# Kernel tuning notes

Measured on AMD Instinct MI355X. Metric: run time of the kernel, lower is better.

Reference implementation:

```python
import jax, jax.numpy as jnp
import numpy as np

EPS = 1e-5  # torch BatchNorm default eps


def _bn(x, gamma, beta, axes):
    # training-mode batch norm over `axes` (channel axis is 1), biased variance as in torch
    mean = x.mean(axis=axes, keepdims=True)
    var = x.var(axis=axes, keepdims=True)
    shp = [1] * x.ndim
    shp[1] = -1
    return gamma.reshape(shp) * (x - mean) * jax.lax.rsqrt(var + EPS) + beta.reshape(shp)


def setup_inputs() -> dict:
    key = jax.random.key(0)
    k0, k1, k2 = jax.random.split(key, 3)
    B, C, H, W = 4, 64, 128, 128
    OP2 = 128      # out_planes * 2
    HEAD = 8       # head_dim
    HP = OP2 // HEAD  # head_planes = 16
    return {
        "x": jax.random.normal(k0, (B, C, H, W), jnp.float32),
        "w_qkv": jax.random.normal(k1, (OP2, C), jnp.float32) / np.sqrt(C).astype(np.float32),
        "gamma1": jnp.ones((OP2,), jnp.float32),
        "beta1": jnp.zeros((OP2,), jnp.float32),
        "pos_relative": jax.random.normal(k2, (HP, 2 * H - 1), jnp.float32) / np.sqrt(C).astype(np.float32),
        "gate_qr": jnp.array([0.1], jnp.float32),
        "gate_kr": jnp.array([0.1], jnp.float32),
        "gate_v_pos": jnp.array([0.1], jnp.float32),
        "gate_v": jnp.array([1.0], jnp.float32),
        "gamma_att": jnp.ones((3 * HEAD,), jnp.float32),
        "beta_att": jnp.zeros((3 * HEAD,), jnp.float32),
        "gamma_v": jnp.ones((2 * HEAD,), jnp.float32),
        "beta_v": jnp.zeros((2 * HEAD,), jnp.float32),
    }


def reference(x, w_qkv, gamma1, beta1, pos_relative, gate_qr, gate_kr,
              gate_v_pos, gate_v, gamma_att, beta_att, gamma_v, beta_v):
    b, c, H, W = x.shape
    # h_w='h': permute [0,3,1,2] -> (b, W, c, H), fuse (b, W)
    xp = jnp.transpose(x, (0, 3, 1, 2)).reshape(b * W, c, H)  # [N, c, H]
    # to_qkv: 1x1 Conv1d (no bias) + ReLU + BatchNorm1d (training mode)
    y = jax.nn.relu(jnp.einsum('oc,ncl->nol', w_qkv, xp))      # [N, 2*out_planes, H]
    y = _bn(y, gamma1, beta1, (0, 2))

    head_dim = gamma_att.shape[0] // 3
    hp = y.shape[1] // head_dim          # head_planes
    qk_dim = hp // 4
    v_dim = hp // 2
    qkv = y.reshape(-1, head_dim, hp, H)  # [N, head_dim, head_planes, H]
    q = qkv[:, :, :qk_dim]
    k = qkv[:, :, qk_dim:2 * qk_dim]
    v = qkv[:, :, 2 * qk_dim:]

    # relative-position gather: pos_relative[:, q_idx - k_idx + H - 1] -> [head_planes, H, H]
    rel = jnp.arange(H)[:, None] - jnp.arange(H)[None, :] + H - 1
    qk_pos = pos_relative[:, rel]
    q_pos = qk_pos[:qk_dim]
    k_pos = qk_pos[qk_dim:2 * qk_dim]
    v_pos = qk_pos[2 * qk_dim:]

    qk = jnp.einsum('nhcp,nhci->nhpi', q, k)                 # [N, head_dim, H, H]
    qr = jnp.einsum('nhcp,cpi->nhpi', q, q_pos) * gate_qr
    kr = jnp.einsum('nhcp,cpi->nhpi', k, k_pos) * gate_kr

    att = _bn(jnp.concatenate([qk, qr, kr], axis=1), gamma_att, beta_att, (0, 2, 3))
    att = att.reshape(-1, 3, head_dim, H, H).sum(axis=1)
    att = jax.nn.softmax(att, axis=-1)

    att_v = jnp.einsum('nhpi,nhci->nhcp', att, v * gate_v)          # [N, head_dim, v_dim, H]
    att_vp = jnp.einsum('nhpi,cpi->nhcp', att, v_pos * gate_v_pos)

    z = _bn(jnp.concatenate([att_v, att_vp], axis=1), gamma_v, beta_v, (0, 2, 3))
    z = z.reshape(b, W, 2, head_dim * v_dim, H).sum(axis=2)  # [b, W, out_planes, H]
    # h_w='h': permute [0,2,3,1] -> (b, out_planes, H, W)
    return jnp.transpose(z, (0, 2, 3, 1))
```

## Files before the change

kernel.cpp:

```cpp
#include <hip/hip_runtime.h>
#include <hip/hip_fp16.h>

#define EPS 1e-5f



typedef _Float16 half2_t __attribute__((ext_vector_type(2)));

__device__ __constant__ int pair_c [10] = {0,0,0,0,1,1,1,2,2,3};
__device__ __constant__ int pair_cp[10] = {0,1,2,3,1,2,3,2,3,3};

__device__ inline float fdot2(half2_t a, half2_t b, float c) {
#if __has_builtin(__builtin_amdgcn_fdot2)
  return __builtin_amdgcn_fdot2(a, b, c, false);
#else
  return c + (float)a[0] * (float)b[0] + (float)a[1] * (float)b[1];
#endif
}
__device__ inline half2_t bch2(unsigned u) {
  union { unsigned u; half2_t h; } x; x.u = u; return x.h;
}
__device__ inline unsigned packf2(float a, float b) {
  half2_t h; h[0] = (_Float16)a; h[1] = (_Float16)b;
  union { unsigned u; half2_t h; } x; x.h = h; return x.u;
}

__global__ __launch_bounds__(256) void k1_gemm(
    const float* __restrict__ x, const float* __restrict__ wq,
    _Float16* __restrict__ y1h, float* __restrict__ Pbuf)
{
  __shared__ float xs[64][132];
  const int b = blockIdx.x >> 7, l = blockIdx.x & 127;
  const int tid = threadIdx.x;
  const float* xp = x + (size_t)b * 1048576 + (size_t)l * 128;
  for (int idx = tid; idx < 8192; idx += 256) {
    int c = idx >> 7, wv = idx & 127;
    xs[c][wv] = xp[c * 16384 + wv];
  }
  __syncthreads();
  const int ty = tid >> 4, tx = tid & 15;
  const int o0 = ty * 8, w0 = tx * 4;
  float acc[8][8];
#pragma unroll
  for (int u = 0; u < 8; ++u)
#pragma unroll
    for (int v = 0; v < 8; ++v) acc[u][v] = 0.f;

  for (int c4 = 0; c4 < 64; c4 += 4) {
    float wr[8][4];
#pragma unroll
    for (int u = 0; u < 8; ++u)
      *(float4*)&wr[u][0] = *(const float4*)&wq[(o0 + u) * 64 + c4];
#pragma unroll
    for (int dc = 0; dc < 4; ++dc) {
      float4 xa = *(const float4*)&xs[c4 + dc][w0];
      float4 xb = *(const float4*)&xs[c4 + dc][w0 + 64];
#pragma unroll
      for (int u = 0; u < 8; ++u) {
        float wv = wr[u][dc];
        acc[u][0] += wv * xa.x; acc[u][1] += wv * xa.y;
        acc[u][2] += wv * xa.z; acc[u][3] += wv * xa.w;
        acc[u][4] += wv * xb.x; acc[u][5] += wv * xb.y;
        acc[u][6] += wv * xb.z; acc[u][7] += wv * xb.w;
      }
    }
  }
  _Float16* y1p = y1h + (size_t)(b * 128 + l) * 16384;
#pragma unroll
  for (int u = 0; u < 8; ++u) {
#pragma unroll
    for (int v = 0; v < 8; ++v) acc[u][v] = fmaxf(acc[u][v], 0.f);
    uint2 pa, pb;
    pa.x = packf2(acc[u][0], acc[u][1]); pa.y = packf2(acc[u][2], acc[u][3]);
    pb.x = packf2(acc[u][4], acc[u][5]); pb.y = packf2(acc[u][6], acc[u][7]);
    *(uint2*)&y1p[(o0 + u) * 128 + w0] = pa;
    *(uint2*)&y1p[(o0 + u) * 128 + w0 + 64] = pb;
    float s  = acc[u][0] + acc[u][1] + acc[u][2] + acc[u][3]
             + acc[u][4] + acc[u][5] + acc[u][6] + acc[u][7];
    float ss = acc[u][0]*acc[u][0] + acc[u][1]*acc[u][1] + acc[u][2]*acc[u][2]
             + acc[u][3]*acc[u][3] + acc[u][4]*acc[u][4] + acc[u][5]*acc[u][5]
             + acc[u][6]*acc[u][6] + acc[u][7]*acc[u][7];
#pragma unroll
    for (int off = 1; off < 16; off <<= 1) {
      s  += __shfl_xor(s, off);
      ss += __shfl_xor(ss, off);
    }
    if (tx == 0) {
      Pbuf[blockIdx.x * 256 + o0 + u] = s;
      Pbuf[blockIdx.x * 256 + 128 + o0 + u] = ss;
    }
  }
}

__global__ __launch_bounds__(64) void k2_bn1(
    const float* __restrict__ Pbuf, float* __restrict__ S,
    const float* __restrict__ g1, const float* __restrict__ b1)
{
  const int t = blockIdx.x;
  const int lane = threadIdx.x;
  float s1 = 0.f, s2 = 0.f;
#pragma unroll
  for (int m = 0; m < 8; ++m) {
    int blk = lane + 64 * m;
    s1 += Pbuf[blk * 256 + t];
    s2 += Pbuf[blk * 256 + 128 + t];
  }
#pragma unroll
  for (int off = 1; off < 64; off <<= 1) {
    s1 += __shfl_xor(s1, off);
    s2 += __shfl_xor(s2, off);
  }
  if (lane == 0) {
    const float inv = 1.f / 65536.f;
    float m = s1 * inv;
    float var = s2 * inv - m * m;
    float sc = g1[t] * rsqrtf(var + EPS);
    S[256 + t] = sc;
    S[384 + t] = b1[t] - m * sc;
  }
}

__global__ __launch_bounds__(256) void k_tr(
    const _Float16* __restrict__ y1h, const float* __restrict__ S,
    unsigned* __restrict__ y2h)
{
  __shared__ _Float16 th[2][64][134];
  const int s = blockIdx.x & 63, b = blockIdx.x >> 6;
  const int h = s >> 3, slot = s & 7;
  const int o0 = 2 * s, o1 = 2 * s + 1;
  const float sc0 = S[256 + o0], sh0 = S[384 + o0];
  const float sc1 = S[256 + o1], sh1 = S[384 + o1];
  const int tid = threadIdx.x;
  for (int lh = 0; lh < 2; ++lh) {
    const int l0 = lh * 64;
    for (int idx = tid; idx < 4096; idx += 256) {
      int ll = idx >> 6, wp = idx & 63;
      size_t base = ((size_t)(b * 128 + l0 + ll) * 128) * 128 + 2 * wp;
      unsigned a0 = *(const unsigned*)&y1h[base + (size_t)o0 * 128];
      unsigned a1 = *(const unsigned*)&y1h[base + (size_t)o1 * 128];
      half2_t ha = bch2(a0), hb = bch2(a1);
      *(unsigned*)&th[0][ll][2 * wp] =
          packf2((float)ha[0] * sc0 + sh0, (float)ha[1] * sc0 + sh0);
      *(unsigned*)&th[1][ll][2 * wp] =
          packf2((float)hb[0] * sc1 + sh1, (float)hb[1] * sc1 + sh1);
    }
    __syncthreads();
    for (int idx = tid; idx < 8192; idx += 256) {
      int w = idx >> 6, ll = idx & 63;
      unsigned pk;
      { half2_t hh; hh[0] = th[0][ll][w]; hh[1] = th[1][ll][w];
        union { unsigned u; half2_t h; } xx; xx.h = hh; pk = xx.u; }
      y2h[((size_t)((b * 128 + w) * 8 + h) * 8 + slot) * 128 + l0 + ll] = pk;
    }
    __syncthreads();
  }
}

__global__ __launch_bounds__(128) void k0_pos(const float* __restrict__ pos,
                                              float* __restrict__ PT,
                                              unsigned* __restrict__ pos_h,
                                              unsigned* __restrict__ vpxg)
{
  const int blk = blockIdx.x, tid = threadIdx.x;
  if (blk == 28) {
    for (int u = tid; u < 255; u += 128) {
#pragma unroll
      for (int s = 0; s < 4; ++s)
        pos_h[u * 4 + s] = packf2(pos[(2 * s) * 255 + u], pos[(2 * s + 1) * 255 + u]);
    }
    return;
  }
  if (blk == 29) {
    for (int m = tid; m < 3072; m += 128) {
      int sel = m / 1536, rem = m % 1536, rp = rem / 12, c = rem % 12;
      unsigned val = 0;
      if (c < 8) {
        int ua = (sel ? 254 : 253) - 2 * rp;
        int ub = ua - 1;
        float fa = (ua >= 0) ? pos[(8 + c) * 255 + ua] : 0.f;
        float fb = (ub >= 0) ? pos[(8 + c) * 255 + ub] : 0.f;
        val = packf2(fa, fb);
      }
      vpxg[m] = val;
    }
    return;
  }
  __shared__ float r0[255], r1[255];
  int rowA, rowB, out;
  bool prod;
  if (blk < 4)       { rowA = blk;                 rowB = rowA;               out = blk * 128;              prod = false; }
  else if (blk < 14) { int m = blk - 4;  rowA = pair_c[m];     rowB = pair_cp[m];     out = 1024 + m * 128; prod = true; }
  else if (blk < 18) { rowA = 4 + (blk - 14);      rowB = rowA;               out = 512 + (blk - 14) * 128; prod = false; }
  else               { int m = blk - 18; rowA = 4 + pair_c[m]; rowB = 4 + pair_cp[m]; out = 2304 + m * 128; prod = true; }
  for (int u = tid; u < 255; u += 128) {
    r0[u] = pos[rowA * 255 + u];
    r1[u] = pos[rowB * 255 + u];
  }
  __syncthreads();
  float s = 0.f;
  if (prod) {
    for (int d = 0; d < 128; ++d) s += r0[tid + d] * r1[tid + d];
  } else {
    for (int d = 0; d < 128; ++d) s += r0[tid + d];
  }
  PT[out + tid] = s;
}

__global__ __launch_bounds__(256) void k3_stats(
    const unsigned* __restrict__ y2h, const float* __restrict__ PT,
    float* __restrict__ Pb3)
{
  const int W = blockIdx.x * 4 + (threadIdx.x >> 6);
  const int lane = threadIdx.x & 63;
  const int h = W & 7;
  const int n0 = (W >> 3) * 8;
  float Pq[4][2], Pk[4][2], Wq[10][2], Wk[10][2];
#pragma unroll
  for (int c = 0; c < 4; ++c) {
    Pq[c][0] = PT[c * 128 + lane];        Pq[c][1] = PT[c * 128 + 64 + lane];
    Pk[c][0] = PT[512 + c * 128 + lane];  Pk[c][1] = PT[512 + c * 128 + 64 + lane];
  }
#pragma unroll
  for (int m = 0; m < 10; ++m) {
    Wq[m][0] = PT[1024 + m * 128 + lane]; Wq[m][1] = PT[1024 + m * 128 + 64 + lane];
    Wk[m][0] = PT[2304 + m * 128 + lane]; Wk[m][1] = PT[2304 + m * 128 + 64 + lane];
  }
  float acc_qk = 0, acc_qkss = 0, acc_qr = 0, acc_qrss = 0, acc_kr = 0, acc_krss = 0;
  for (int t = 0; t < 8; ++t) {
    const unsigned* yb = y2h + (size_t)((n0 + t) * 8 + h) * 1024;
    float q[4][2], k[4][2];
#pragma unroll
    for (int pl = 0; pl < 2; ++pl) {
      half2_t ha = bch2(yb[pl * 128 + lane]);
      half2_t hb = bch2(yb[pl * 128 + 64 + lane]);
      q[2 * pl][0] = (float)ha[0]; q[2 * pl + 1][0] = (float)ha[1];
      q[2 * pl][1] = (float)hb[0]; q[2 * pl + 1][1] = (float)hb[1];
      half2_t hc = bch2(yb[(2 + pl) * 128 + lane]);
      half2_t hd = bch2(yb[(2 + pl) * 128 + 64 + lane]);
      k[2 * pl][0] = (float)hc[0]; k[2 * pl + 1][0] = (float)hc[1];
      k[2 * pl][1] = (float)hd[0]; k[2 * pl + 1][1] = (float)hd[1];
    }
#pragma unroll
    for (int c = 0; c < 4; ++c) {
      acc_qr += q[c][0] * Pq[c][0] + q[c][1] * Pq[c][1];
      acc_kr += k[c][0] * Pk[c][0] + k[c][1] * Pk[c][1];
    }
#pragma unroll
    for (int m = 0; m < 10; ++m) {
      int c = pair_c[m], cp = pair_cp[m];
      float mult = (c == cp) ? 1.f : 2.f;
      acc_qrss += mult * (q[c][0] * q[cp][0] * Wq[m][0] + q[c][1] * q[cp][1] * Wq[m][1]);
      acc_krss += mult * (k[c][0] * k[cp][0] * Wk[m][0] + k[c][1] * k[cp][1] * Wk[m][1]);
    }
    float vals[28];
#pragma unroll
    for (int c = 0; c < 4; ++c) {
      vals[c]     = q[c][0] + q[c][1];
      vals[4 + c] = k[c][0] + k[c][1];
    }
#pragma unroll
    for (int m = 0; m < 10; ++m) {
      int c = pair_c[m], cp = pair_cp[m];
      vals[8 + m]  = q[c][0] * q[cp][0] + q[c][1] * q[cp][1];
      vals[18 + m] = k[c][0] * k[cp][0] + k[c][1] * k[cp][1];
    }
#pragma unroll
    for (int v = 0; v < 28; ++v) {
      float tv = vals[v];
#pragma unroll
      for (int off = 1; off < 64; off <<= 1) tv += __shfl_xor(tv, off);
      vals[v] = tv;
    }
    float qk = 0, qkss = 0;
#pragma unroll
    for (int c = 0; c < 4; ++c) qk += vals[c] * vals[4 + c];
#pragma unroll
    for (int m = 0; m < 10; ++m) {
      float mult = (pair_c[m] == pair_cp[m]) ? 1.f : 2.f;
      qkss += mult * vals[8 + m] * vals[18 + m];
    }
    acc_qk += qk; acc_qkss += qkss;
  }
  float lin[4] = {acc_qr, acc_qrss, acc_kr, acc_krss};
#pragma unroll
  for (int v = 0; v < 4; ++v) {
    float tv = lin[v];
#pragma unroll
    for (int off = 1; off < 64; off <<= 1) tv += __shfl_xor(tv, off);
    lin[v] = tv;
  }
  if (lane == 0) {
    float* o = Pb3 + W * 6;
    o[0] = acc_qk; o[1] = acc_qkss;
    o[2] = lin[0]; o[3] = lin[1]; o[4] = lin[2]; o[5] = lin[3];
  }
}

__global__ __launch_bounds__(64) void kR1(
    const float* __restrict__ Pb3, float* __restrict__ S,
    const float* __restrict__ ga, const float* __restrict__ ba,
    const float* __restrict__ gqr, const float* __restrict__ gkr)
{
  __shared__ float sums[48];
  const int t = threadIdx.x;
  if (t < 48) {
    int h = t / 6, k = t % 6;
    float v = 0.f;
    for (int g = 0; g < 64; ++g) v += Pb3[(h + 8 * g) * 6 + k];
    sums[t] = v;
  }
  __syncthreads();
  if (t < 8) {
    const int h = t;
    const float inv = 1.f / 8388608.f;
    float gates[3] = {1.f, gqr[0], gkr[0]};
    float csum = 0.f;
#pragma unroll
    for (int g = 0; g < 3; ++g) {
      float mr = sums[h * 6 + 2 * g] * inv;
      float er = sums[h * 6 + 2 * g + 1] * inv;
      float gt = gates[g];
      float mean = gt * mr;
      float var = gt * gt * er - mean * mean;
      float sc = ga[g * 8 + h] * rsqrtf(var + EPS);
      S[560 + g * 8 + h] = gt * sc;
      csum += ba[g * 8 + h] - mean * sc;
    }
    S[584 + h] = csum;
  }
}

__global__ __launch_bounds__(512, 6) void k5_apply(
    const unsigned* __restrict__ y2h, const unsigned* __restrict__ pos_h,
    const unsigned* __restrict__ vpxg,
    float* __restrict__ S, _Float16* __restrict__ av, _Float16* __restrict__ avp,
    const float* __restrict__ gv_p, const float* __restrict__ gvp_p,
    float* __restrict__ Vbuf)
{
  __shared__ __align__(16) unsigned qkv_s[128][4];
  __shared__ __align__(16) unsigned posm[255][4];
  __shared__ __align__(16) unsigned vt[64][8];
  __shared__ __align__(16) unsigned vpx[2][128][12];
  __shared__ float red[8][4];
  const int h = blockIdx.x & 7, n = blockIdx.x >> 3;
  const int tid = threadIdx.x;
  const unsigned* yb = y2h + (size_t)(n * 8 + h) * 1024;
  {
    int l = tid >> 2, s = tid & 3;
    qkv_s[l][s] = yb[s * 128 + l];
  }
  {
    unsigned* pf = (unsigned*)posm;
    for (int m = tid; m < 1020; m += 512) pf[m] = pos_h[m];
  }
  {
    unsigned* pf = (unsigned*)vpx;
    for (int m = tid; m < 3072; m += 512) pf[m] = vpxg[m];
  }
  if (tid < 256) {
    int s = tid & 3, jp = tid >> 2;
    unsigned a0 = yb[(4 + s) * 128 + 2 * jp];
    unsigned a1 = yb[(4 + s) * 128 + 2 * jp + 1];
    vt[jp][2 * s]     = (a0 & 0xffffu) | (a1 << 16);
    vt[jp][2 * s + 1] = (a0 >> 16) | (a1 & 0xffff0000u);
  }
  __syncthreads();

  const int p = tid >> 2, isub = tid & 3;
  uint2 qk2 = *(const uint2*)&qkv_s[p][0];
  uint2 kown = *(const uint2*)&qkv_s[p][2];
  const half2_t q01 = bch2(qk2.x), q23 = bch2(qk2.y);
  const half2_t k01o = bch2(kown.x), k23o = bch2(kown.y);
  const float C0 = S[560 + h], C1 = S[568 + h], C2 = S[576 + h], C3v = S[584 + h];
  const unsigned* vprow = &vpx[p & 1][63 - (p >> 1)][0];

  float mcur = -1e30f;
  float sum = 0.f;
  float accv[8], accvp[8];
#pragma unroll
  for (int c = 0; c < 8; ++c) { accv[c] = 0.f; accvp[c] = 0.f; }

#pragma unroll 4
  for (int j = 0; j < 16; ++j) {
    const int jp = isub + 4 * j;
    const int i0 = 2 * jp;
    const int u0 = p - i0 + 127;
    uint2 ka = *(const uint2*)&qkv_s[i0][2];
    uint2 kb = *(const uint2*)&qkv_s[i0 + 1][2];
    uint4 pa = *(const uint4*)&posm[u0][0];
    uint4 pb = *(const uint4*)&posm[u0 - 1][0];
    float aa0 = fdot2(q23, bch2(ka.y), fdot2(q01, bch2(ka.x), 0.f));
    float bq0 = fdot2(q23, bch2(pa.y), fdot2(q01, bch2(pa.x), 0.f));
    float ckA = fdot2(k23o, bch2(pa.w), fdot2(k01o, bch2(pa.z), 0.f));
    float aa1 = fdot2(q23, bch2(kb.y), fdot2(q01, bch2(kb.x), 0.f));
    float bq1 = fdot2(q23, bch2(pb.y), fdot2(q01, bch2(pb.x), 0.f));
    float ckB = fdot2(k23o, bch2(pb.w), fdot2(k01o, bch2(pb.z), 0.f));
    float s0 = aa0 * C0 + bq0 * C1 + ckA * C2 + C3v;
    float s1 = aa1 * C0 + bq1 * C1 + ckB * C2 + C3v;
    float mp = fmaxf(s0, s1);
    if (mp > mcur) {
      float r = __expf(mcur - mp);
      mcur = mp;
      sum *= r;
#pragma unroll
      for (int c = 0; c < 8; ++c) { accv[c] *= r; accvp[c] *= r; }
    }
    float e0 = __expf(s0 - mcur);
    float e1 = __expf(s1 - mcur);
    sum += e0 + e1;
    const half2_t e2 = bch2(packf2(e0, e1));
    uint4 va = *(const uint4*)&vt[jp][0];
    uint4 vb = *(const uint4*)&vt[jp][4];
    const unsigned* wr = vprow + jp * 12;
    uint4 wa = *(const uint4*)wr;
    uint4 wb = *(const uint4*)(wr + 4);
    accv[0] = fdot2(e2, bch2(va.x), accv[0]);
    accv[1] = fdot2(e2, bch2(va.y), accv[1]);
    accv[2] = fdot2(e2, bch2(va.z), accv[2]);
    accv[3] = fdot2(e2, bch2(va.w), accv[3]);
    accv[4] = fdot2(e2, bch2(vb.x), accv[4]);
    accv[5] = fdot2(e2, bch2(vb.y), accv[5]);
    accv[6] = fdot2(e2, bch2(vb.z), accv[6]);
    accv[7] = fdot2(e2, bch2(vb.w), accv[7]);
    accvp[0] = fdot2(e2, bch2(wa.x), accvp[0]);
    accvp[1] = fdot2(e2, bch2(wa.y), accvp[1]);
    accvp[2] = fdot2(e2, bch2(wa.z), accvp[2]);
    accvp[3] = fdot2(e2, bch2(wa.w), accvp[3]);
    accvp[4] = fdot2(e2, bch2(wb.x), accvp[4]);
    accvp[5] = fdot2(e2, bch2(wb.y), accvp[5]);
    accvp[6] = fdot2(e2, bch2(wb.z), accvp[6]);
    accvp[7] = fdot2(e2, bch2(wb.w), accvp[7]);
  }
  float M = fmaxf(mcur, __shfl_xor(mcur, 1));
  M = fmaxf(M, __shfl_xor(M, 2));
  {
    float r = __expf(mcur - M);
    sum *= r;
#pragma unroll
    for (int c = 0; c < 8; ++c) { accv[c] *= r; accvp[c] *= r; }
  }
  sum += __shfl_xor(sum, 1);
  sum += __shfl_xor(sum, 2);
#pragma unroll
  for (int c = 0; c < 8; ++c) {
    accv[c]  += __shfl_xor(accv[c], 1);  accv[c]  += __shfl_xor(accv[c], 2);
    accvp[c] += __shfl_xor(accvp[c], 1); accvp[c] += __shfl_xor(accvp[c], 2);
  }

  float sv = 0, ssv = 0, svp = 0, ssvp = 0;
  if (isub == 0) {
    const float fv = gv_p[0] / sum, fp2 = gvp_p[0] / sum;
    size_t base = ((size_t)(n * 8 + h) * 8) * 128 + p;
#pragma unroll
    for (int c = 0; c < 8; ++c) {
      float x1 = accv[c] * fv;
      float x2 = accvp[c] * fp2;
      av [base + c * 128] = (_Float16)x1;
      avp[base + c * 128] = (_Float16)x2;
      sv += x1; ssv += x1 * x1; svp += x2; ssvp += x2 * x2;
    }
  }
  float vals[4] = {sv, ssv, svp, ssvp};
#pragma unroll
  for (int kk = 0; kk < 4; ++kk) {
    float v = vals[kk];
#pragma unroll
    for (int off = 1; off < 64; off <<= 1) v += __shfl_xor(v, off);
    vals[kk] = v;
  }
  const int wid = tid >> 6, lane = tid & 63;
  if (lane == 0) {
#pragma unroll
    for (int kk = 0; kk < 4; ++kk) red[wid][kk] = vals[kk];
  }
  __syncthreads();
  if (tid == 0) {
    float t0 = 0, t1 = 0, t2 = 0, t3 = 0;
#pragma unroll
    for (int w = 0; w < 8; ++w) {
      t0 += red[w][0]; t1 += red[w][1]; t2 += red[w][2]; t3 += red[w][3];
    }
    float* o = Vbuf + (size_t)blockIdx.x * 4;
    o[0] = t0; o[1] = t1; o[2] = t2; o[3] = t3;
  }
}

__global__ __launch_bounds__(512) void kR2(
    const float* __restrict__ Vbuf, float* __restrict__ S,
    const float* __restrict__ gv, const float* __restrict__ bv)
{
  __shared__ float part[32][17];
  const int t = threadIdx.x;
  const int col = t >> 4, sub = t & 15;
  const int k = col >> 3, h = col & 7;
  float v = 0.f;
  for (int m = 0; m < 32; ++m) {
    int n = sub + 16 * m;
    v += Vbuf[(size_t)(n * 8 + h) * 4 + k];
  }
  part[col][sub] = v;
  __syncthreads();
  if (t < 32) {
    float s = 0.f;
#pragma unroll
    for (int j = 0; j < 16; ++j) s += part[t][j];
    part[t][16] = s;
  }
  __syncthreads();
  if (t < 8) {
    const int hh = t;
    const float inv = 1.f / 524288.f;
    float m1 = part[0 * 8 + hh][16] * inv;
    float e1 = part[1 * 8 + hh][16] * inv;
    float var = e1 - m1 * m1;
    float sc = gv[hh] * rsqrtf(var + EPS);
    S[624 + hh] = sc;
    S[632 + hh] = bv[hh] - m1 * sc;
    float m2 = part[2 * 8 + hh][16] * inv;
    float e2 = part[3 * 8 + hh][16] * inv;
    var = e2 - m2 * m2;
    sc = gv[8 + hh] * rsqrtf(var + EPS);
    S[640 + hh] = sc;
    S[648 + hh] = bv[8 + hh] - m2 * sc;
  }
}

__global__ __launch_bounds__(256) void k7_out(
    const _Float16* __restrict__ av, const _Float16* __restrict__ avp,
    const float* __restrict__ S, float* __restrict__ out)
{
  __shared__ float tile[64][129];
  const int wt = blockIdx.x & 1;
  const int d  = (blockIdx.x >> 1) & 63;
  const int b  = blockIdx.x >> 7;
  const int h = d >> 3, c = d & 7;
  const float scv = S[624 + h], shv = S[632 + h];
  const float scp = S[640 + h], shp = S[648 + h];
  const int tid = threadIdx.x;
  for (int idx = tid; idx < 8192; idx += 256) {
    int wl = idx >> 7, pp = idx & 127;
    int n = b * 128 + wt * 64 + wl;
    size_t base = (((size_t)n * 8 + h) * 8 + c) * 128 + pp;
    tile[wl][pp] = (float)av[base] * scv + shv + (float)avp[base] * scp + shp;
  }
  __syncthreads();
  for (int idx = tid; idx < 8192; idx += 256) {
    int pp = idx >> 6, wl = idx & 63;
    out[(((size_t)b * 64 + d) * 128 + pp) * 128 + wt * 64 + wl] = tile[wl][pp];
  }
}

extern "C" void kernel_launch(void* const* d_in, const int* in_sizes, int n_in,
                              void* d_out, int out_size, void* d_ws, size_t ws_size,
                              hipStream_t stream)
{
  const float* x   = (const float*)d_in[0];
  const float* wq  = (const float*)d_in[1];
  const float* g1  = (const float*)d_in[2];
  const float* b1  = (const float*)d_in[3];
  const float* pos = (const float*)d_in[4];
  const float* gqr = (const float*)d_in[5];
  const float* gkr = (const float*)d_in[6];
  const float* gvp = (const float*)d_in[7];
  const float* gv  = (const float*)d_in[8];
  const float* ga  = (const float*)d_in[9];
  const float* ba  = (const float*)d_in[10];
  const float* gv2 = (const float*)d_in[11];
  const float* bv2 = (const float*)d_in[12];

  float* ws = (float*)d_ws;
  _Float16* y1h   = (_Float16*)ws;
  _Float16* av    = (_Float16*)ws;
  _Float16* avp   = (_Float16*)ws + 4194304;
  float*    Pb3   = ws + 4200000;
  float*    Vbuf  = ws + 4250000;
  float*    Pbuf  = ws + 8388608;
  unsigned* y2h   = (unsigned*)(ws + 8388608);
  float*    S     = ws + 16777216;
  unsigned* pos_h = (unsigned*)(ws + 16778240);
  float*    PT    = ws + 16781312;
  unsigned* vpxg  = (unsigned*)(ws + 16785000);
  float*    out   = (float*)d_out;

  k0_pos<<<30, 128, 0, stream>>>(pos, PT, pos_h, vpxg);
  k1_gemm<<<512, 256, 0, stream>>>(x, wq, y1h, Pbuf);
  k2_bn1<<<128, 64, 0, stream>>>(Pbuf, S, g1, b1);
  k_tr<<<256, 256, 0, stream>>>(y1h, S, y2h);
  k3_stats<<<128, 256, 0, stream>>>(y2h, PT, Pb3);
  kR1<<<1, 64, 0, stream>>>(Pb3, S, ga, ba, gqr, gkr);
  k5_apply<<<4096, 512, 0, stream>>>(y2h, pos_h, vpxg, S, av, avp, gv, gvp, Vbuf);
  kR2<<<1, 512, 0, stream>>>(Vbuf, S, gv2, bv2);
  k7_out<<<512, 256, 0, stream>>>(av, avp, S, out);
}
```

Before: 215.7 us.

## Fuse BN1 finalize into transpose, vectorize x loads, widen softmax inner loop

Removes the separate k2_bn1 launch: each k_tr block now reduces the BN1 partial sums for its two channels itself and computes scale and shift locally. Pbuf is moved to a different workspace offset, presumably so it no longer overlaps y2h, which k_tr now writes while still reading Pbuf. The k1_gemm shared-memory fill now uses float4 loads, and the k5_apply attention loop handles four scores per iteration with paired fdot2 accumulation and a dot-with-ones for the running sum. The trade is redundant BN1 reductions across the 4 batch blocks per channel pair and higher register pressure in the fully unrolled attention loop.

```diff
diff --git a/kernel.cpp b/kernel.cpp
--- a/kernel.cpp
+++ b/kernel.cpp
@@ -33,9 +33,9 @@
   const int b = blockIdx.x >> 7, l = blockIdx.x & 127;
   const int tid = threadIdx.x;
   const float* xp = x + (size_t)b * 1048576 + (size_t)l * 128;
-  for (int idx = tid; idx < 8192; idx += 256) {
-    int c = idx >> 7, wv = idx & 127;
-    xs[c][wv] = xp[c * 16384 + wv];
+  for (int idx = tid; idx < 2048; idx += 256) {
+    int c = idx >> 5, w4 = (idx & 31) * 4;
+    *(float4*)&xs[c][w4] = *(const float4*)&xp[c * 16384 + w4];
   }
   __syncthreads();
   const int ty = tid >> 4, tx = tid & 15;
@@ -92,45 +92,33 @@
   }
 }
 
-__global__ __launch_bounds__(64) void k2_bn1(
-    const float* __restrict__ Pbuf, float* __restrict__ S,
-    const float* __restrict__ g1, const float* __restrict__ b1)
-{
-  const int t = blockIdx.x;
-  const int lane = threadIdx.x;
-  float s1 = 0.f, s2 = 0.f;
-#pragma unroll
-  for (int m = 0; m < 8; ++m) {
-    int blk = lane + 64 * m;
-    s1 += Pbuf[blk * 256 + t];
-    s2 += Pbuf[blk * 256 + 128 + t];
-  }
-#pragma unroll
-  for (int off = 1; off < 64; off <<= 1) {
-    s1 += __shfl_xor(s1, off);
-    s2 += __shfl_xor(s2, off);
-  }
-  if (lane == 0) {
-    const float inv = 1.f / 65536.f;
-    float m = s1 * inv;
-    float var = s2 * inv - m * m;
-    float sc = g1[t] * rsqrtf(var + EPS);
-    S[256 + t] = sc;
-    S[384 + t] = b1[t] - m * sc;
-  }
-}
-
 __global__ __launch_bounds__(256) void k_tr(
-    const _Float16* __restrict__ y1h, const float* __restrict__ S,
+    const _Float16* __restrict__ y1h, const float* __restrict__ Pbuf,
+    const float* __restrict__ g1, const float* __restrict__ b1,
     unsigned* __restrict__ y2h)
 {
   __shared__ _Float16 th[2][64][134];
+  __shared__ float scsh[4];
   const int s = blockIdx.x & 63, b = blockIdx.x >> 6;
   const int h = s >> 3, slot = s & 7;
   const int o0 = 2 * s, o1 = 2 * s + 1;
-  const float sc0 = S[256 + o0], sh0 = S[384 + o0];
-  const float sc1 = S[256 + o1], sh1 = S[384 + o1];
   const int tid = threadIdx.x;
+  {
+    int r = tid >> 6, lane = tid & 63;
+    int row = ((r & 1) ? o1 : o0) + (r >> 1) * 128;
+    float a = 0.f;
+#pragma unroll
+    for (int m = 0; m < 8; ++m) a += Pbuf[(lane + 64 * m) * 256 + row];
+#pragma unroll
+    for (int off = 1; off < 64; off <<= 1) a += __shfl_xor(a, off);
+    if (lane == 0) scsh[r] = a;
+  }
+  __syncthreads();
+  const float inv = 1.f / 65536.f;
+  const float m0 = scsh[0] * inv, v0 = scsh[2] * inv - m0 * m0;
+  const float m1 = scsh[1] * inv, v1 = scsh[3] * inv - m1 * m1;
+  const float sc0 = g1[o0] * rsqrtf(v0 + EPS), sh0 = b1[o0] - m0 * sc0;
+  const float sc1 = g1[o1] * rsqrtf(v1 + EPS), sh1 = b1[o1] - m1 * sc1;
   for (int lh = 0; lh < 2; ++lh) {
     const int l0 = lh * 64;
     for (int idx = tid; idx < 4096; idx += 256) {
@@ -373,6 +361,7 @@
   const half2_t k01o = bch2(kown.x), k23o = bch2(kown.y);
   const float C0 = S[560 + h], C1 = S[568 + h], C2 = S[576 + h], C3v = S[584 + h];
   const unsigned* vprow = &vpx[p & 1][63 - (p >> 1)][0];
+  const half2_t one2 = bch2(packf2(1.f, 1.f));
 
   float mcur = -1e30f;
   float sum = 0.f;
@@ -380,24 +369,34 @@
 #pragma unroll
   for (int c = 0; c < 8; ++c) { accv[c] = 0.f; accvp[c] = 0.f; }
 
-#pragma unroll 4
-  for (int j = 0; j < 16; ++j) {
-    const int jp = isub + 4 * j;
-    const int i0 = 2 * jp;
-    const int u0 = p - i0 + 127;
-    uint2 ka = *(const uint2*)&qkv_s[i0][2];
-    uint2 kb = *(const uint2*)&qkv_s[i0 + 1][2];
-    uint4 pa = *(const uint4*)&posm[u0][0];
-    uint4 pb = *(const uint4*)&posm[u0 - 1][0];
-    float aa0 = fdot2(q23, bch2(ka.y), fdot2(q01, bch2(ka.x), 0.f));
-    float bq0 = fdot2(q23, bch2(pa.y), fdot2(q01, bch2(pa.x), 0.f));
-    float ckA = fdot2(k23o, bch2(pa.w), fdot2(k01o, bch2(pa.z), 0.f));
-    float aa1 = fdot2(q23, bch2(kb.y), fdot2(q01, bch2(kb.x), 0.f));
-    float bq1 = fdot2(q23, bch2(pb.y), fdot2(q01, bch2(pb.x), 0.f));
-    float ckB = fdot2(k23o, bch2(pb.w), fdot2(k01o, bch2(pb.z), 0.f));
-    float s0 = aa0 * C0 + bq0 * C1 + ckA * C2 + C3v;
-    float s1 = aa1 * C0 + bq1 * C1 + ckB * C2 + C3v;
-    float mp = fmaxf(s0, s1);
+#pragma unroll
+  for (int jj = 0; jj < 8; ++jj) {
+    const int jpA = isub + 8 * jj;
+    const int jpB = jpA + 4;
+    const int i0A = 2 * jpA, i0B = 2 * jpB;
+    const int uA = p - i0A + 127;
+    const int uB = uA - 8;
+    uint2 kaA = *(const uint2*)&qkv_s[i0A][2];
+    uint2 kbA = *(const uint2*)&qkv_s[i0A + 1][2];
+    uint2 kaB = *(const uint2*)&qkv_s[i0B][2];
+    uint2 kbB = *(const uint2*)&qkv_s[i0B + 1][2];
+    uint4 paA = *(const uint4*)&posm[uA][0];
+    uint4 pbA = *(const uint4*)&posm[uA - 1][0];
+    uint4 paB = *(const uint4*)&posm[uB][0];
+    uint4 pbB = *(const uint4*)&posm[uB - 1][0];
+    float s0 = fdot2(q23, bch2(kaA.y), fdot2(q01, bch2(kaA.x), 0.f)) * C0
+             + fdot2(q23, bch2(paA.y), fdot2(q01, bch2(paA.x), 0.f)) * C1
+             + fdot2(k23o, bch2(paA.w), fdot2(k01o, bch2(paA.z), 0.f)) * C2 + C3v;
+    float s1 = fdot2(q23, bch2(kbA.y), fdot2(q01, bch2(kbA.x), 0.f)) * C0
+             + fdot2(q23, bch2(pbA.y), fdot2(q01, bch2(pbA.x), 0.f)) * C1
+             + fdot2(k23o, bch2(pbA.w), fdot2(k01o, bch2(pbA.z), 0.f)) * C2 + C3v;
+    float s2 = fdot2(q23, bch2(kaB.y), fdot2(q01, bch2(kaB.x), 0.f)) * C0
+             + fdot2(q23, bch2(paB.y), fdot2(q01, bch2(paB.x), 0.f)) * C1
+             + fdot2(k23o, bch2(paB.w), fdot2(k01o, bch2(paB.z), 0.f)) * C2 + C3v;
+    float s3 = fdot2(q23, bch2(kbB.y), fdot2(q01, bch2(kbB.x), 0.f)) * C0
+             + fdot2(q23, bch2(pbB.y), fdot2(q01, bch2(pbB.x), 0.f)) * C1
+             + fdot2(k23o, bch2(pbB.w), fdot2(k01o, bch2(pbB.z), 0.f)) * C2 + C3v;
+    float mp = fmaxf(fmaxf(s0, s1), fmaxf(s2, s3));
     if (mp > mcur) {
       float r = __expf(mcur - mp);
       mcur = mp;
@@ -407,29 +406,37 @@
     }
     float e0 = __expf(s0 - mcur);
     float e1 = __expf(s1 - mcur);
-    sum += e0 + e1;
-    const half2_t e2 = bch2(packf2(e0, e1));
-    uint4 va = *(const uint4*)&vt[jp][0];
-    uint4 vb = *(const uint4*)&vt[jp][4];
-    const unsigned* wr = vprow + jp * 12;
-    uint4 wa = *(const uint4*)wr;
-    uint4 wb = *(const uint4*)(wr + 4);
-    accv[0] = fdot2(e2, bch2(va.x), accv[0]);
-    accv[1] = fdot2(e2, bch2(va.y), accv[1]);
-    accv[2] = fdot2(e2, bch2(va.z), accv[2]);
-    accv[3] = fdot2(e2, bch2(va.w), accv[3]);
-    accv[4] = fdot2(e2, bch2(vb.x), accv[4]);
-    accv[5] = fdot2(e2, bch2(vb.y), accv[5]);
-    accv[6] = fdot2(e2, bch2(vb.z), accv[6]);
-    accv[7] = fdot2(e2, bch2(vb.w), accv[7]);
-    accvp[0] = fdot2(e2, bch2(wa.x), accvp[0]);
-    accvp[1] = fdot2(e2, bch2(wa.y), accvp[1]);
-    accvp[2] = fdot2(e2, bch2(wa.z), accvp[2]);
-    accvp[3] = fdot2(e2, bch2(wa.w), accvp[3]);
-    accvp[4] = fdot2(e2, bch2(wb.x), accvp[4]);
-    accvp[5] = fdot2(e2, bch2(wb.y), accvp[5]);
-    accvp[6] = fdot2(e2, bch2(wb.z), accvp[6]);
-    accvp[7] = fdot2(e2, bch2(wb.w), accvp[7]);
+    float e2f = __expf(s2 - mcur);
+    float e3f = __expf(s3 - mcur);
+    const half2_t eA = bch2(packf2(e0, e1));
+    const half2_t eB = bch2(packf2(e2f, e3f));
+    sum = fdot2(eB, one2, fdot2(eA, one2, sum));
+    uint4 vaA = *(const uint4*)&vt[jpA][0];
+    uint4 vbA = *(const uint4*)&vt[jpA][4];
+    uint4 vaB = *(const uint4*)&vt[jpB][0];
+    uint4 vbB = *(const uint4*)&vt[jpB][4];
+    const unsigned* wrA = vprow + jpA * 12;
+    const unsigned* wrB = vprow + jpB * 12;
+    uint4 waA = *(const uint4*)wrA;
+    uint4 wbA = *(const uint4*)(wrA + 4);
+    uint4 waB = *(const uint4*)wrB;
+    uint4 wbB = *(const uint4*)(wrB + 4);
+    accv[0] = fdot2(eB, bch2(vaB.x), fdot2(eA, bch2(vaA.x), accv[0]));
+    accv[1] = fdot2(eB, bch2(vaB.y), fdot2(eA, bch2(vaA.y), accv[1]));
+    accv[2] = fdot2(eB, bch2(vaB.z), fdot2(eA, bch2(vaA.z), accv[2]));
+    accv[3] = fdot2(eB, bch2(vaB.w), fdot2(eA, bch2(vaA.w), accv[3]));
+    accv[4] = fdot2(eB, bch2(vbB.x), fdot2(eA, bch2(vbA.x), accv[4]));
+    accv[5] = fdot2(eB, bch2(vbB.y), fdot2(eA, bch2(vbA.y), accv[5]));
+    accv[6] = fdot2(eB, bch2(vbB.z), fdot2(eA, bch2(vbA.z), accv[6]));
+    accv[7] = fdot2(eB, bch2(vbB.w), fdot2(eA, bch2(vbA.w), accv[7]));
+    accvp[0] = fdot2(eB, bch2(waB.x), fdot2(eA, bch2(waA.x), accvp[0]));
+    accvp[1] = fdot2(eB, bch2(waB.y), fdot2(eA, bch2(waA.y), accvp[1]));
+    accvp[2] = fdot2(eB, bch2(waB.z), fdot2(eA, bch2(waA.z), accvp[2]));
+    accvp[3] = fdot2(eB, bch2(waB.w), fdot2(eA, bch2(waA.w), accvp[3]));
+    accvp[4] = fdot2(eB, bch2(wbB.x), fdot2(eA, bch2(wbA.x), accvp[4]));
+    accvp[5] = fdot2(eB, bch2(wbB.y), fdot2(eA, bch2(wbA.y), accvp[5]));
+    accvp[6] = fdot2(eB, bch2(wbB.z), fdot2(eA, bch2(wbA.z), accvp[6]));
+    accvp[7] = fdot2(eB, bch2(wbB.w), fdot2(eA, bch2(wbA.w), accvp[7]));
   }
   float M = fmaxf(mcur, __shfl_xor(mcur, 1));
   M = fmaxf(M, __shfl_xor(M, 2));
@@ -574,7 +581,7 @@
   _Float16* avp   = (_Float16*)ws + 4194304;
   float*    Pb3   = ws + 4200000;
   float*    Vbuf  = ws + 4250000;
-  float*    Pbuf  = ws + 8388608;
+  float*    Pbuf  = ws + 4300000;
   unsigned* y2h   = (unsigned*)(ws + 8388608);
   float*    S     = ws + 16777216;
   unsigned* pos_h = (unsigned*)(ws + 16778240);
@@ -584,8 +591,7 @@
 
   k0_pos<<<30, 128, 0, stream>>>(pos, PT, pos_h, vpxg);
   k1_gemm<<<512, 256, 0, stream>>>(x, wq, y1h, Pbuf);
-  k2_bn1<<<128, 64, 0, stream>>>(Pbuf, S, g1, b1);
-  k_tr<<<256, 256, 0, stream>>>(y1h, S, y2h);
+  k_tr<<<256, 256, 0, stream>>>(y1h, Pbuf, g1, b1, y2h);
   k3_stats<<<128, 256, 0, stream>>>(y2h, PT, Pb3);
   kR1<<<1, 64, 0, stream>>>(Pb3, S, ga, ba, gqr, gkr);
   k5_apply<<<4096, 512, 0, stream>>>(y2h, pos_h, vpxg, S, av, avp, gv, gvp, Vbuf);
```

Measured after the change: 209.9 us. 2.7% less time.
